# Kernel tuning notes

Hardware: AMD Instinct MI355X
Metric: run time of the kernel (lower is better)

The kernel has to match this reference:

```python
import jax, jax.numpy as jnp
import numpy as np


def setup_inputs() -> dict:
    key = jax.random.key(0)
    k1, = jax.random.split(key, 1)
    inputs = jax.random.normal(k1, (16, 64, 64, 512), dtype=jnp.float32)
    gamma = jnp.zeros((1,), dtype=jnp.float32)
    return {"inputs": inputs, "gamma": gamma}


def reference(inputs, gamma):
    # inputs: [B, H, W, C] (NHWC)
    B, H, W, C = inputs.shape
    vec_a = inputs.reshape(B, H * W, C)              # [B, N, C], N = H*W
    # channel Gram matrix: aTa[b, i, j] = sum_n a[b, n, i] * a[b, n, j]
    aTa = jnp.einsum('bni,bnj->bij', vec_a, vec_a)    # [B, C, C]
    attn = jax.nn.softmax(aTa, axis=-1)               # softmax over last axis
    # aaTa = attn @ vec_a^T -> [B, C, N]; transpose -> [B, N, C]
    aaTa = jnp.einsum('bij,bnj->bni', attn, vec_a)    # [B, N, C]
    aaTa = aaTa.reshape(B, H, W, C)
    return gamma * aaTa + inputs
```

## Files before the change

kernel.cpp:

```cpp
#include <hip/hip_runtime.h>

#define BATCH 16
#define NPIX  4096
#define CCH   512
#define NSPLIT 8
#define KSPL  (NPIX / NSPLIT)
#define NUT   10

using bf16x8   = __attribute__((ext_vector_type(8))) __bf16;
using floatx4  = __attribute__((ext_vector_type(4))) float;
using ushort8v = __attribute__((ext_vector_type(8))) unsigned short;
using ushort4v = __attribute__((ext_vector_type(4))) unsigned short;

static __device__ __forceinline__ unsigned short f2bf(float f) {
    unsigned u = __builtin_bit_cast(unsigned, f);
    unsigned r = 0x7fffu + ((u >> 16) & 1u);
    return (unsigned short)((u + r) >> 16);
}
static __device__ __forceinline__ float bf2f(unsigned short v) {
    unsigned u = ((unsigned)v) << 16;
    return __builtin_bit_cast(float, u);
}
static __device__ __forceinline__ bf16x8 ld_frag(const unsigned short* p) {
    return __builtin_bit_cast(bf16x8, *(const ushort8v*)p);
}
static __device__ __forceinline__ void gld16(const unsigned short* g, unsigned short* l) {
    __builtin_amdgcn_global_load_lds(
        (const __attribute__((address_space(1))) void*)g,
        (__attribute__((address_space(3))) void*)l,
        16, 0, 0);
}

__global__ __launch_bounds__(256) void k_cvt(const float* __restrict__ inp,
                                             unsigned short* __restrict__ Abf,
                                             unsigned short* __restrict__ AT) {
    __shared__ unsigned short sN[64 * 66];
    const int bn = blockIdx.x, bc = blockIdx.y, b = blockIdx.z;
    const int t  = threadIdx.x;
    const int n0 = bn * 64, c0 = bc * 64;
    const float* ip = inp + ((size_t)b * NPIX + n0) * CCH + c0;
    unsigned short* op = Abf + ((size_t)b * NPIX + n0) * CCH + c0;

#pragma unroll
    for (int r = 0; r < 2; ++r) {
        int n  = r * 32 + (t >> 3);
        int c8 = (t & 7) * 8;
        float4 v0 = *(const float4*)(ip + (size_t)n * CCH + c8);
        float4 v1 = *(const float4*)(ip + (size_t)n * CCH + c8 + 4);
        ushort8v w;
        w[0] = f2bf(v0.x); w[1] = f2bf(v0.y); w[2] = f2bf(v0.z); w[3] = f2bf(v0.w);
        w[4] = f2bf(v1.x); w[5] = f2bf(v1.y); w[6] = f2bf(v1.z); w[7] = f2bf(v1.w);
        *(ushort8v*)(op + (size_t)n * CCH + c8) = w;
        *(ushort8v*)&sN[n * 66 + c8] = w;
    }
    __syncthreads();

    const int cp = t >> 3;
    const int ng = (t & 7) * 8;
    ushort8v o0, o1;
#pragma unroll
    for (int k = 0; k < 8; ++k) {
        unsigned d = *(const unsigned*)&sN[(ng + k) * 66 + cp * 2];
        o0[k] = (unsigned short)(d & 0xffffu);
        o1[k] = (unsigned short)(d >> 16);
    }
    unsigned short* tp = AT + ((size_t)b * CCH + c0) * NPIX + n0;
    *(ushort8v*)(tp + (size_t)(cp * 2)     * NPIX + ng) = o0;
    *(ushort8v*)(tp + (size_t)(cp * 2 + 1) * NPIX + ng) = o1;
}

__global__ __launch_bounds__(256) void k_ata(const unsigned short* __restrict__ AT,
                                             unsigned short* __restrict__ Sp) {
    __shared__ unsigned short sA0[128 * 32];
    __shared__ unsigned short sA1[128 * 32];
    __shared__ unsigned short sB0[128 * 32];
    __shared__ unsigned short sB1[128 * 32];
    const int orig = blockIdx.x + gridDim.x * (blockIdx.y + gridDim.y * blockIdx.z);
    const int swz  = (orig & 7) * (NUT * NSPLIT * BATCH / 8) + (orig >> 3);
    const int u = swz % NUT;
    const int s = (swz / NUT) % NSPLIT;
    const int b = swz / (NUT * NSPLIT);

    const int ti = (u < 4) ? 0 : (u < 7) ? 1 : (u < 9) ? 2 : 3;
    const int u0 = ti * 5 - (ti * (ti + 1)) / 2;
    const int tj = ti + (u - u0);
    const unsigned short* pa = AT + ((size_t)b * CCH + ti * 128) * NPIX + s * KSPL;
    const unsigned short* pb = AT + ((size_t)b * CCH + tj * 128) * NPIX + s * KSPL;
    const int tid = threadIdx.x, lane = tid & 63, wave = tid >> 6;
    const int lrow = lane >> 2;
    const int lk   = (lane & 3) * 8;

    floatx4 acc[2][8];
#pragma unroll
    for (int tm = 0; tm < 2; ++tm)
#pragma unroll
        for (int tn = 0; tn < 8; ++tn)
            acc[tm][tn] = floatx4{0.f, 0.f, 0.f, 0.f};

#define ATA_STAGE(DA, DB, K0)                                                  \
    {                                                                          \
        _Pragma("unroll")                                                      \
        for (int i = 0; i < 2; ++i) {                                          \
            const int r = wave * 32 + i * 16;                                  \
            gld16(pa + (size_t)(r + lrow) * NPIX + (K0) + lk, &DA[r * 32]);    \
            gld16(pb + (size_t)(r + lrow) * NPIX + (K0) + lk, &DB[r * 32]);    \
        }                                                                      \
    }

#define ATA_COMP(SA, SB)                                                       \
    {                                                                          \
        const int kq = (lane >> 4) * 8;                                        \
        bf16x8 af[2], bv[8];                                                   \
        _Pragma("unroll")                                                      \
        for (int tm = 0; tm < 2; ++tm)                                         \
            af[tm] = ld_frag(&SA[(wave * 32 + tm * 16 + (lane & 15)) * 32 + kq]); \
        _Pragma("unroll")                                                      \
        for (int tn = 0; tn < 8; ++tn)                                         \
            bv[tn] = ld_frag(&SB[(tn * 16 + (lane & 15)) * 32 + kq]);          \
        _Pragma("unroll")                                                      \
        for (int tm = 0; tm < 2; ++tm)                                         \
            _Pragma("unroll")                                                  \
            for (int tn = 0; tn < 8; ++tn)                                     \
                acc[tm][tn] = __builtin_amdgcn_mfma_f32_16x16x32_bf16(         \
                    af[tm], bv[tn], acc[tm][tn], 0, 0, 0);                     \
    }

    ATA_STAGE(sA0, sB0, 0)
    __syncthreads();

    for (int t = 0; t < KSPL / 32; t += 2) {
        ATA_STAGE(sA1, sB1, (t + 1) * 32)
        ATA_COMP(sA0, sB0)
        __syncthreads();
        if (t + 2 < KSPL / 32) ATA_STAGE(sA0, sB0, (t + 2) * 32)
        ATA_COMP(sA1, sB1)
        __syncthreads();
    }
#undef ATA_STAGE
#undef ATA_COMP

    unsigned short* Tb = Sp + ((((size_t)s * BATCH + b) * NUT + u) << 14);
#pragma unroll
    for (int tm = 0; tm < 2; ++tm)
#pragma unroll
        for (int tn = 0; tn < 8; ++tn) {
            ushort4v w;
#pragma unroll
            for (int r = 0; r < 4; ++r) w[r] = f2bf(acc[tm][tn][r]);
            *(ushort4v*)&Tb[((((wave * 2 + tm) * 8 + tn) * 64) + lane) * 4] = w;
        }
}

__global__ __launch_bounds__(256) void k_softmax(const unsigned short* __restrict__ Sp,
                                                 unsigned short* __restrict__ P) {
    __shared__ float red[6];
    const int row = blockIdx.x;
    const int b = row >> 9, i = row & 511;
    const int tid = threadIdx.x, lane = tid & 63, wave = tid >> 6;
    const size_t sstr = (size_t)BATCH * NUT * 16384;

    float x[2];
#pragma unroll
    for (int e = 0; e < 2; ++e) {
        const int j  = tid + e * 256;
        const int ti = i >> 7, tj = j >> 7;
        const int il = i & 127, jl = j & 127;
        const bool sw = ti > tj;
        const int a  = sw ? tj : ti;
        const int cm = sw ? ti : tj;
        const int u  = a * 4 + cm - ((a * (a + 1)) >> 1);
        const int rr = sw ? jl : il;
        const int cc = sw ? il : jl;
        const int off = ((((rr >> 4) * 8 + (cc >> 4)) * 64) +
                         ((rr >> 2) & 3) * 16 + (cc & 15)) * 4 + (rr & 3);
        const size_t base = (((size_t)b * NUT + u) << 14) + off;
        float v = 0.f;
#pragma unroll
        for (int s = 0; s < NSPLIT; ++s) v += bf2f(Sp[base + s * sstr]);
        x[e] = v;
    }

    float m = fmaxf(x[0], x[1]);
#pragma unroll
    for (int o = 32; o; o >>= 1) m = fmaxf(m, __shfl_xor(m, o, 64));
    if (lane == 0) red[wave] = m;
    __syncthreads();
    if (tid == 0) red[4] = fmaxf(fmaxf(red[0], red[1]), fmaxf(red[2], red[3]));
    __syncthreads();
    m = red[4];

    float e0 = __expf(x[0] - m), e1 = __expf(x[1] - m);
    float sum = e0 + e1;
#pragma unroll
    for (int o = 32; o; o >>= 1) sum += __shfl_xor(sum, o, 64);
    if (lane == 0) red[wave] = sum;
    __syncthreads();
    if (tid == 0) red[5] = red[0] + red[1] + red[2] + red[3];
    __syncthreads();
    float inv = 1.0f / red[5];

    P[(size_t)row * CCH + tid]       = f2bf(e0 * inv);
    P[(size_t)row * CCH + tid + 256] = f2bf(e1 * inv);
}

__global__ __launch_bounds__(256) void k_av(const unsigned short* __restrict__ Abf,
                                            const unsigned short* __restrict__ P,
                                            const float* __restrict__ inp,
                                            const float* __restrict__ gamma,
                                            float* __restrict__ out) {
    __shared__ unsigned short sA0[128 * 32];
    __shared__ unsigned short sA1[128 * 32];
    __shared__ unsigned short sB0[128 * 32];
    __shared__ unsigned short sB1[128 * 32];
    const int orig = blockIdx.x + gridDim.x * (blockIdx.y + gridDim.y * blockIdx.z);
    const int swz  = (orig & 7) * ((NPIX / 128) * (CCH / 128) * BATCH / 8) + (orig >> 3);
    const int bn = swz % (NPIX / 128);
    const int bi = (swz / (NPIX / 128)) % (CCH / 128);
    const int b  = swz / ((NPIX / 128) * (CCH / 128));

    const unsigned short* pa = Abf + ((size_t)b * NPIX + bn * 128) * CCH;
    const unsigned short* pb = P + ((size_t)b * CCH + bi * 128) * CCH;
    const int tid = threadIdx.x, lane = tid & 63, wave = tid >> 6;
    const int lrow = lane >> 2;
    const int lk   = (lane & 3) * 8;
    const float g = gamma[0];

    floatx4 acc[2][8];
#pragma unroll
    for (int tm = 0; tm < 2; ++tm)
#pragma unroll
        for (int tn = 0; tn < 8; ++tn)
            acc[tm][tn] = floatx4{0.f, 0.f, 0.f, 0.f};

#define AV_STAGE(DA, DB, K0)                                                   \
    {                                                                          \
        _Pragma("unroll")                                                      \
        for (int i = 0; i < 2; ++i) {                                          \
            const int r = wave * 32 + i * 16;                                  \
            gld16(pa + (size_t)(r + lrow) * CCH + (K0) + lk, &DA[r * 32]);     \
            gld16(pb + (size_t)(r + lrow) * CCH + (K0) + lk, &DB[r * 32]);     \
        }                                                                      \
    }

#define AV_COMP(SA, SB)                                                        \
    {                                                                          \
        const int kq = (lane >> 4) * 8;                                        \
        bf16x8 af[2], bv[8];                                                   \
        _Pragma("unroll")                                                      \
        for (int tm = 0; tm < 2; ++tm)                                         \
            af[tm] = ld_frag(&SA[(wave * 32 + tm * 16 + (lane & 15)) * 32 + kq]); \
        _Pragma("unroll")                                                      \
        for (int tn = 0; tn < 8; ++tn)                                         \
            bv[tn] = ld_frag(&SB[(tn * 16 + (lane & 15)) * 32 + kq]);          \
        _Pragma("unroll")                                                      \
        for (int tm = 0; tm < 2; ++tm)                                         \
            _Pragma("unroll")                                                  \
            for (int tn = 0; tn < 8; ++tn)                                     \
                acc[tm][tn] = __builtin_amdgcn_mfma_f32_16x16x32_bf16(         \
                    af[tm], bv[tn], acc[tm][tn], 0, 0, 0);                     \
    }

    AV_STAGE(sA0, sB0, 0)
    __syncthreads();

    for (int t = 0; t < CCH / 32; t += 2) {
        AV_STAGE(sA1, sB1, (t + 1) * 32)
        AV_COMP(sA0, sB0)
        __syncthreads();
        if (t + 2 < CCH / 32) AV_STAGE(sA0, sB0, (t + 2) * 32)
        AV_COMP(sA1, sB1)
        __syncthreads();
    }
#undef AV_STAGE
#undef AV_COMP

    float* Ob = out + ((size_t)b * NPIX + bn * 128) * CCH + bi * 128;
    const float* Ib = inp + ((size_t)b * NPIX + bn * 128) * CCH + bi * 128;
#pragma unroll
    for (int tm = 0; tm < 2; ++tm)
#pragma unroll
        for (int tn = 0; tn < 8; ++tn)
#pragma unroll
            for (int r = 0; r < 4; ++r) {
                int nrow = wave * 32 + tm * 16 + (lane >> 4) * 4 + r;
                int icol = tn * 16 + (lane & 15);
                size_t o = (size_t)nrow * CCH + icol;
                Ob[o] = g * acc[tm][tn][r] + Ib[o];
            }
}

extern "C" void kernel_launch(void* const* d_in, const int* in_sizes, int n_in,
                              void* d_out, int out_size, void* d_ws, size_t ws_size,
                              hipStream_t stream) {
    const float* inp   = (const float*)d_in[0];
    const float* gamma = (const float*)d_in[1];
    float* out = (float*)d_out;

    char* ws = (char*)d_ws;
    unsigned short* Abf = (unsigned short*)ws;
    unsigned short* AT  = (unsigned short*)(ws + (size_t)67108864);
    unsigned short* Sp  = (unsigned short*)(ws + (size_t)134217728);
    unsigned short* P   = (unsigned short*)(ws + (size_t)134217728 + 41943040);

    k_cvt<<<dim3(NPIX / 64, CCH / 64, BATCH), 256, 0, stream>>>(inp, Abf, AT);
    k_ata<<<dim3(NUT, NSPLIT, BATCH), 256, 0, stream>>>(AT, Sp);
    k_softmax<<<BATCH * CCH, 256, 0, stream>>>(Sp, P);
    k_av<<<dim3(NPIX / 128, CCH / 128, BATCH), 256, 0, stream>>>(Abf, P, inp, gamma, out);
}
```

Baseline: 461.6 us.

## Triple-buffer GEMM LDS staging with vmcnt-based waits and inline ds_read

Both GEMM kernels (Gram and attention-apply) move from a double-buffered LDS pipeline with full __syncthreads to a fully unrolled triple-buffered pipeline. It waits with s_waitcnt vmcnt(4) plus a raw s_barrier, so two tile loads stay in flight while one tile is computed. Fragment reads become inline-asm ds_read_b128 with immediate offsets, followed by an explicit lgkmcnt wait and a sched_barrier. The block-index swizzle for L2 locality is removed and plain grid indices are used instead. The cost is more LDS per block, which may lower occupancy, plus a less predictable L2 access order.

```diff
diff --git a/kernel.cpp b/kernel.cpp
--- a/kernel.cpp
+++ b/kernel.cpp
@@ -21,15 +21,14 @@
     unsigned u = ((unsigned)v) << 16;
     return __builtin_bit_cast(float, u);
 }
-static __device__ __forceinline__ bf16x8 ld_frag(const unsigned short* p) {
-    return __builtin_bit_cast(bf16x8, *(const ushort8v*)p);
-}
 static __device__ __forceinline__ void gld16(const unsigned short* g, unsigned short* l) {
     __builtin_amdgcn_global_load_lds(
         (const __attribute__((address_space(1))) void*)g,
         (__attribute__((address_space(3))) void*)l,
         16, 0, 0);
 }
+#define LOFF(p) ((unsigned)(unsigned long long)(__attribute__((address_space(3))) const void*)(p))
+#define DSR(d, a, o) asm volatile("ds_read_b128 %0, %1 offset:" o : "=v"(d) : "v"(a))
 
 __global__ __launch_bounds__(256) void k_cvt(const float* __restrict__ inp,
                                              unsigned short* __restrict__ Abf,
@@ -69,18 +68,40 @@
     *(ushort8v*)(tp + (size_t)(cp * 2 + 1) * NPIX + ng) = o1;
 }
 
+#define GEMM_COMP(AADR, BADR)                                                  \
+    {                                                                          \
+        bf16x8 af[2], bv[8];                                                   \
+        DSR(af[0], (AADR), "0");    DSR(af[1], (AADR), "1024");                \
+        DSR(bv[0], (BADR), "0");    DSR(bv[1], (BADR), "1024");                \
+        DSR(bv[2], (BADR), "2048"); DSR(bv[3], (BADR), "3072");                \
+        DSR(bv[4], (BADR), "4096"); DSR(bv[5], (BADR), "5120");                \
+        DSR(bv[6], (BADR), "6144"); DSR(bv[7], (BADR), "7168");                \
+        asm volatile("s_waitcnt lgkmcnt(0)" ::: "memory");                     \
+        __builtin_amdgcn_sched_barrier(0);                                     \
+        _Pragma("unroll")                                                      \
+        for (int tm = 0; tm < 2; ++tm)                                         \
+            _Pragma("unroll")                                                  \
+            for (int tn = 0; tn < 8; ++tn)                                     \
+                acc[tm][tn] = __builtin_amdgcn_mfma_f32_16x16x32_bf16(         \
+                    af[tm], bv[tn], acc[tm][tn], 0, 0, 0);                     \
+    }
+
+#define GEMM_WAIT4                                                             \
+    asm volatile("s_waitcnt vmcnt(4)" ::: "memory");                           \
+    __builtin_amdgcn_s_barrier();
+#define GEMM_WAIT0                                                             \
+    asm volatile("s_waitcnt vmcnt(0)" ::: "memory");                           \
+    __builtin_amdgcn_s_barrier();
+
 __global__ __launch_bounds__(256) void k_ata(const unsigned short* __restrict__ AT,
                                              unsigned short* __restrict__ Sp) {
     __shared__ unsigned short sA0[128 * 32];
     __shared__ unsigned short sA1[128 * 32];
+    __shared__ unsigned short sA2[128 * 32];
     __shared__ unsigned short sB0[128 * 32];
     __shared__ unsigned short sB1[128 * 32];
-    const int orig = blockIdx.x + gridDim.x * (blockIdx.y + gridDim.y * blockIdx.z);
-    const int swz  = (orig & 7) * (NUT * NSPLIT * BATCH / 8) + (orig >> 3);
-    const int u = swz % NUT;
-    const int s = (swz / NUT) % NSPLIT;
-    const int b = swz / (NUT * NSPLIT);
-
+    __shared__ unsigned short sB2[128 * 32];
+    const int u = blockIdx.x, s = blockIdx.y, b = blockIdx.z;
     const int ti = (u < 4) ? 0 : (u < 7) ? 1 : (u < 9) ? 2 : 3;
     const int u0 = ti * 5 - (ti * (ti + 1)) / 2;
     const int tj = ti + (u - u0);
@@ -89,6 +110,12 @@
     const int tid = threadIdx.x, lane = tid & 63, wave = tid >> 6;
     const int lrow = lane >> 2;
     const int lk   = (lane & 3) * 8;
+    const int kq   = (lane >> 4) * 8;
+
+    const unsigned aoff = (unsigned)((wave * 32 + (lane & 15)) * 64 + kq * 2);
+    const unsigned boff = (unsigned)((lane & 15) * 64 + kq * 2);
+    const unsigned aA0 = LOFF(sA0) + aoff, aA1 = LOFF(sA1) + aoff, aA2 = LOFF(sA2) + aoff;
+    const unsigned aB0 = LOFF(sB0) + boff, aB1 = LOFF(sB1) + boff, aB2 = LOFF(sB2) + boff;
 
     floatx4 acc[2][8];
 #pragma unroll
@@ -97,7 +124,7 @@
         for (int tn = 0; tn < 8; ++tn)
             acc[tm][tn] = floatx4{0.f, 0.f, 0.f, 0.f};
 
-#define ATA_STAGE(DA, DB, K0)                                                  \
+#define STG(DA, DB, K0)                                                        \
     {                                                                          \
         _Pragma("unroll")                                                      \
         for (int i = 0; i < 2; ++i) {                                          \
@@ -106,38 +133,30 @@
             gld16(pb + (size_t)(r + lrow) * NPIX + (K0) + lk, &DB[r * 32]);    \
         }                                                                      \
     }
-
-#define ATA_COMP(SA, SB)                                                       \
-    {                                                                          \
-        const int kq = (lane >> 4) * 8;                                        \
-        bf16x8 af[2], bv[8];                                                   \
-        _Pragma("unroll")                                                      \
-        for (int tm = 0; tm < 2; ++tm)                                         \
-            af[tm] = ld_frag(&SA[(wave * 32 + tm * 16 + (lane & 15)) * 32 + kq]); \
-        _Pragma("unroll")                                                      \
-        for (int tn = 0; tn < 8; ++tn)                                         \
-            bv[tn] = ld_frag(&SB[(tn * 16 + (lane & 15)) * 32 + kq]);          \
-        _Pragma("unroll")                                                      \
-        for (int tm = 0; tm < 2; ++tm)                                         \
-            _Pragma("unroll")                                                  \
-            for (int tn = 0; tn < 8; ++tn)                                     \
-                acc[tm][tn] = __builtin_amdgcn_mfma_f32_16x16x32_bf16(         \
-                    af[tm], bv[tn], acc[tm][tn], 0, 0, 0);                     \
-    }
-
-    ATA_STAGE(sA0, sB0, 0)
-    __syncthreads();
-
-    for (int t = 0; t < KSPL / 32; t += 2) {
-        ATA_STAGE(sA1, sB1, (t + 1) * 32)
-        ATA_COMP(sA0, sB0)
-        __syncthreads();
-        if (t + 2 < KSPL / 32) ATA_STAGE(sA0, sB0, (t + 2) * 32)
-        ATA_COMP(sA1, sB1)
-        __syncthreads();
-    }
-#undef ATA_STAGE
-#undef ATA_COMP
+#define BODYS(NA, NB, K2, CA, CB) STG(NA, NB, K2) GEMM_COMP(CA, CB) GEMM_WAIT4
+
+    STG(sA0, sB0, 0)
+    STG(sA1, sB1, 32)
+    GEMM_WAIT4
+
+    BODYS(sA2, sB2,  64, aA0, aB0)
+    BODYS(sA0, sB0,  96, aA1, aB1)
+    BODYS(sA1, sB1, 128, aA2, aB2)
+    BODYS(sA2, sB2, 160, aA0, aB0)
+    BODYS(sA0, sB0, 192, aA1, aB1)
+    BODYS(sA1, sB1, 224, aA2, aB2)
+    BODYS(sA2, sB2, 256, aA0, aB0)
+    BODYS(sA0, sB0, 288, aA1, aB1)
+    BODYS(sA1, sB1, 320, aA2, aB2)
+    BODYS(sA2, sB2, 352, aA0, aB0)
+    BODYS(sA0, sB0, 384, aA1, aB1)
+    BODYS(sA1, sB1, 416, aA2, aB2)
+    BODYS(sA2, sB2, 448, aA0, aB0)
+    BODYS(sA0, sB0, 480, aA1, aB1)
+    GEMM_COMP(aA2, aB2) GEMM_WAIT0
+    GEMM_COMP(aA0, aB0)
+#undef BODYS
+#undef STG
 
     unsigned short* Tb = Sp + ((((size_t)s * BATCH + b) * NUT + u) << 14);
 #pragma unroll
@@ -210,20 +229,23 @@
                                             float* __restrict__ out) {
     __shared__ unsigned short sA0[128 * 32];
     __shared__ unsigned short sA1[128 * 32];
+    __shared__ unsigned short sA2[128 * 32];
     __shared__ unsigned short sB0[128 * 32];
     __shared__ unsigned short sB1[128 * 32];
-    const int orig = blockIdx.x + gridDim.x * (blockIdx.y + gridDim.y * blockIdx.z);
-    const int swz  = (orig & 7) * ((NPIX / 128) * (CCH / 128) * BATCH / 8) + (orig >> 3);
-    const int bn = swz % (NPIX / 128);
-    const int bi = (swz / (NPIX / 128)) % (CCH / 128);
-    const int b  = swz / ((NPIX / 128) * (CCH / 128));
-
+    __shared__ unsigned short sB2[128 * 32];
+    const int bn = blockIdx.x, bi = blockIdx.y, b = blockIdx.z;
     const unsigned short* pa = Abf + ((size_t)b * NPIX + bn * 128) * CCH;
     const unsigned short* pb = P + ((size_t)b * CCH + bi * 128) * CCH;
     const int tid = threadIdx.x, lane = tid & 63, wave = tid >> 6;
     const int lrow = lane >> 2;
     const int lk   = (lane & 3) * 8;
+    const int kq   = (lane >> 4) * 8;
     const float g = gamma[0];
+
+    const unsigned aoff = (unsigned)((wave * 32 + (lane & 15)) * 64 + kq * 2);
+    const unsigned boff = (unsigned)((lane & 15) * 64 + kq * 2);
+    const unsigned aA0 = LOFF(sA0) + aoff, aA1 = LOFF(sA1) + aoff, aA2 = LOFF(sA2) + aoff;
+    const unsigned aB0 = LOFF(sB0) + boff, aB1 = LOFF(sB1) + boff, aB2 = LOFF(sB2) + boff;
 
     floatx4 acc[2][8];
 #pragma unroll
@@ -232,7 +254,7 @@
         for (int tn = 0; tn < 8; ++tn)
             acc[tm][tn] = floatx4{0.f, 0.f, 0.f, 0.f};
 
-#define AV_STAGE(DA, DB, K0)                                                   \
+#define STG(DA, DB, K0)                                                        \
     {                                                                          \
         _Pragma("unroll")                                                      \
         for (int i = 0; i < 2; ++i) {                                          \
@@ -241,38 +263,30 @@
             gld16(pb + (size_t)(r + lrow) * CCH + (K0) + lk, &DB[r * 32]);     \
         }                                                                      \
     }
-
-#define AV_COMP(SA, SB)                                                        \
-    {                                                                          \
-        const int kq = (lane >> 4) * 8;                                        \
-        bf16x8 af[2], bv[8];                                                   \
-        _Pragma("unroll")                                                      \
-        for (int tm = 0; tm < 2; ++tm)                                         \
-            af[tm] = ld_frag(&SA[(wave * 32 + tm * 16 + (lane & 15)) * 32 + kq]); \
-        _Pragma("unroll")                                                      \
-        for (int tn = 0; tn < 8; ++tn)                                         \
-            bv[tn] = ld_frag(&SB[(tn * 16 + (lane & 15)) * 32 + kq]);          \
-        _Pragma("unroll")                                                      \
-        for (int tm = 0; tm < 2; ++tm)                                         \
-            _Pragma("unroll")                                                  \
-            for (int tn = 0; tn < 8; ++tn)                                     \
-                acc[tm][tn] = __builtin_amdgcn_mfma_f32_16x16x32_bf16(         \
-                    af[tm], bv[tn], acc[tm][tn], 0, 0, 0);                     \
-    }
-
-    AV_STAGE(sA0, sB0, 0)
-    __syncthreads();
-
-    for (int t = 0; t < CCH / 32; t += 2) {
-        AV_STAGE(sA1, sB1, (t + 1) * 32)
-        AV_COMP(sA0, sB0)
-        __syncthreads();
-        if (t + 2 < CCH / 32) AV_STAGE(sA0, sB0, (t + 2) * 32)
-        AV_COMP(sA1, sB1)
-        __syncthreads();
-    }
-#undef AV_STAGE
-#undef AV_COMP
+#define BODYS(NA, NB, K2, CA, CB) STG(NA, NB, K2) GEMM_COMP(CA, CB) GEMM_WAIT4
+
+    STG(sA0, sB0, 0)
+    STG(sA1, sB1, 32)
+    GEMM_WAIT4
+
+    BODYS(sA2, sB2,  64, aA0, aB0)
+    BODYS(sA0, sB0,  96, aA1, aB1)
+    BODYS(sA1, sB1, 128, aA2, aB2)
+    BODYS(sA2, sB2, 160, aA0, aB0)
+    BODYS(sA0, sB0, 192, aA1, aB1)
+    BODYS(sA1, sB1, 224, aA2, aB2)
+    BODYS(sA2, sB2, 256, aA0, aB0)
+    BODYS(sA0, sB0, 288, aA1, aB1)
+    BODYS(sA1, sB1, 320, aA2, aB2)
+    BODYS(sA2, sB2, 352, aA0, aB0)
+    BODYS(sA0, sB0, 384, aA1, aB1)
+    BODYS(sA1, sB1, 416, aA2, aB2)
+    BODYS(sA2, sB2, 448, aA0, aB0)
+    BODYS(sA0, sB0, 480, aA1, aB1)
+    GEMM_COMP(aA2, aB2) GEMM_WAIT0
+    GEMM_COMP(aA0, aB0)
+#undef BODYS
+#undef STG
 
     float* Ob = out + ((size_t)b * NPIX + bn * 128) * CCH + bi * 128;
     const float* Ib = inp + ((size_t)b * NPIX + bn * 128) * CCH + bi * 128;
```

After: 406.2 us. -12.0%, faster.
